# Kernel optimization log

Hardware: AMD Instinct MI355X
Metric: run time of the kernel (lower is better)

Reference implementation:

```python
import jax, jax.numpy as jnp
import numpy as np

N, G, E, B, H = 20000, 32768, 1_000_000, 64, 128

def _lin_w(k, fan_in, fan_out):
    return jax.random.normal(k, (fan_in, fan_out), jnp.float32) / np.sqrt(fan_in)

def setup_inputs() -> dict:
    key = jax.random.key(0)
    ks = jax.random.split(key, 12)
    node_embedding = jax.random.normal(ks[0], (N, H), jnp.float32)
    node_pos = jax.random.uniform(ks[1], (N, 3), jnp.float32)
    grid_pos = jax.random.uniform(ks[2], (G, 3), jnp.float32)
    index_i = jax.random.randint(ks[3], (E,), 0, N, jnp.int32)
    index_j = jax.random.randint(ks[4], (E,), N, N + G, jnp.int32)  # grid ids offset by N
    edge_index = jnp.stack([index_i, index_j], axis=0)
    # orthonormal per-graph frames via QR for realism
    q, _ = jnp.linalg.qr(jax.random.normal(ks[5], (B, 3, 3), jnp.float32))
    batch = jnp.sort(jax.random.randint(ks[6], (N,), 0, B, jnp.int32))
    wk = jax.random.split(ks[7], 6)
    return {
        "node_embedding": node_embedding, "node_pos": node_pos, "grid_pos": grid_pos,
        "edge_index": edge_index, "equi_frames": q, "batch": batch,
        "We1": _lin_w(wk[0], 3, H), "be1": jnp.zeros((H,), jnp.float32),
        "We2": _lin_w(wk[1], H, H), "be2": jnp.zeros((H,), jnp.float32),
        "Wm1": _lin_w(wk[2], 2 * H, H), "bm1": jnp.zeros((H,), jnp.float32),
        "Wm2": _lin_w(wk[3], H, H), "bm2": jnp.zeros((H,), jnp.float32),
        "Wu1": _lin_w(wk[4], H, H), "bu1": jnp.zeros((H,), jnp.float32),
        "Wu2": _lin_w(wk[5], H, H), "bu2": jnp.zeros((H,), jnp.float32),
    }

def _mlp(x, W1, b1, W2, b2):
    return jax.nn.silu(x @ W1 + b1) @ W2 + b2

def reference(node_embedding, node_pos, grid_pos, edge_index, equi_frames, batch,
              We1, be1, We2, be2, Wm1, bm1, Wm2, bm2, Wu1, bu1, Wu2, bu2):
    n_nodes = node_pos.shape[0]
    n_seg = n_nodes + grid_pos.shape[0]
    i, j = edge_index[0], edge_index[1]
    # per-edge gathers
    rel_pos = grid_pos[j - n_nodes] - node_pos[i]          # [E,3]
    frames = equi_frames[batch[i]]                          # [E,3,3]
    local_rel = jnp.einsum('eab,eb->ea', frames, rel_pos)   # frame bmm
    pos_emb = _mlp(local_rel, We1, be1, We2, be2)           # [E,H]
    msg = jnp.concatenate([node_embedding[i], pos_emb], -1) # [E,2H]
    msg = _mlp(msg, Wm1, bm1, Wm2, bm2)                     # [E,H]
    # scatter-mean over destination (grid) index; segments [0,N) receive none
    seg_sum = jax.ops.segment_sum(msg, j, num_segments=n_seg)
    cnt = jax.ops.segment_sum(jnp.ones((j.shape[0],), msg.dtype), j, num_segments=n_seg)
    mean = seg_sum / jnp.maximum(cnt, 1.0)[:, None]         # safe div (torch gives NaN on empty)
    return _mlp(mean, Wu1, bu1, Wu2, bu2)                   # [N+G, H]
```

## Files before the change

### kernel.cpp

```cpp
#include <hip/hip_runtime.h>
#include <hip/hip_fp16.h>

#define HN 128
#define NN 20000
#define GG 32768
#define EE 1000000
#define NSEG (NN + GG)
#define TE 128

typedef _Float16 f16;
typedef __attribute__((ext_vector_type(8))) _Float16 f16x8;
typedef __attribute__((ext_vector_type(4))) float f32x4;

__device__ __forceinline__ int swz_h(int row, int col) {
  int b = (row << 8) + (col << 1);
  b ^= (row & 7) << 4;
  return b >> 1;
}

__device__ __forceinline__ int swz_f(int row, int lcol) {
  int b = (row << 8) + (lcol << 2);
  b ^= (row & 7) << 4;
  return b >> 2;
}

__device__ __forceinline__ float silu_f(float x) {
  return x / (1.0f + __expf(-x));
}

__device__ __forceinline__ f32x4 mfma16(f16x8 a, f16x8 b, f32x4 c) {
  return __builtin_amdgcn_mfma_f32_16x16x32_f16(a, b, c, 0, 0, 0);
}

__global__ void pack_weights(const float* __restrict__ Wm1,
                             const float* __restrict__ Wm2,
                             const float* __restrict__ Wu1,
                             const float* __restrict__ Wu2,
                             f16* __restrict__ dst) {
  int p = blockIdx.x * 256 + threadIdx.x;
  if (p >= 81920) return;
  const float* src; int K, off, q;
  if (p < 32768)      { src = Wm1; K = 256; off = 0;     q = p; }
  else if (p < 49152) { src = Wm2; K = 128; off = 32768; q = p - 32768; }
  else if (p < 65536) { src = Wu1; K = 128; off = 49152; q = p - 49152; }
  else                { src = Wu2; K = 128; off = 65536; q = p - 65536; }
  int KS = K >> 5;
  int t   = q / (KS * 512);
  int rem = q - t * KS * 512;
  int s   = rem >> 9;
  int qq  = rem & 511;
  int lane = qq >> 3, e = qq & 7;
  int k = s * 32 + ((lane >> 4) << 3) + e;
  int n = (t << 4) + (lane & 15);
  dst[off + q] = (f16)src[k * HN + n];
}

__global__ void wc_vec_kernel(const float* __restrict__ We2,
                              const float* __restrict__ Wm1,
                              const float* __restrict__ be2,
                              const float* __restrict__ bm1,
                              const float* __restrict__ bu1,
                              const float* __restrict__ Wu2,
                              const float* __restrict__ bu2,
                              f16* __restrict__ Wcp,
                              float* __restrict__ bvec,
                              float* __restrict__ cvec) {
  if (blockIdx.x < 64) {
    int o = blockIdx.x * 256 + threadIdx.x;
    int k = o >> 7, n = o & 127;
    float s = 0.0f;
    for (int m = 0; m < 128; m++)
      s += We2[k * HN + m] * Wm1[(128 + m) * HN + n];
    int t = n >> 4, sg = k >> 5;
    int lane = (((k >> 3) & 3) << 4) | (n & 15);
    int e = k & 7;
    Wcp[((size_t)(t * 4 + sg) * 64 + lane) * 8 + e] = (f16)s;
  } else {
    int tid = threadIdx.x;
    if (tid < 128) {
      float s = bm1[tid];
      for (int m = 0; m < 128; m++) s += be2[m] * Wm1[(128 + m) * HN + tid];
      bvec[tid] = s;
    } else {
      int n = tid - 128;
      float s = bu2[n];
      for (int m = 0; m < 128; m++) s += silu_f(bu1[m]) * Wu2[m * HN + n];
      cvec[n] = s;
    }
  }
}

__global__ __launch_bounds__(256, 2) void ynode_kernel(
    const float* __restrict__ emb, const f16* __restrict__ Wm1p,
    const float* __restrict__ bvec, f16* __restrict__ Ynode) {
  __shared__ __align__(16) f16 A1[TE * HN];
  const int tid = threadIdx.x;
  const int rbase = blockIdx.x * TE;

  for (int idx = tid; idx < TE * HN; idx += 256) {
    int e = idx >> 7, h = idx & (HN - 1);
    int row = rbase + e;
    float v = (row < NN) ? emb[(size_t)row * HN + h] : 0.0f;
    A1[swz_h(e, h)] = (f16)v;
  }
  __syncthreads();

  const int lane = tid & 63;
  const int w = tid >> 6;
  const int lr_ = lane & 15;
  const int hi = lane >> 4;
  const int r0w = w * 32;

  f16x8 a[2][4];
#pragma unroll
  for (int mt = 0; mt < 2; mt++)
#pragma unroll
    for (int s = 0; s < 4; s++)
      a[mt][s] = *(const f16x8*)(A1 + swz_h(r0w + mt * 16 + lr_, s * 32 + hi * 8));

  f32x4 acc[2][8];
#pragma unroll
  for (int t = 0; t < 8; t++) {
    float bv = bvec[t * 16 + lr_];
    acc[0][t] = (f32x4){bv, bv, bv, bv};
    acc[1][t] = (f32x4){bv, bv, bv, bv};
  }
#pragma unroll
  for (int t = 0; t < 8; t++)
#pragma unroll
    for (int s = 0; s < 4; s++) {
      f16x8 b = *(const f16x8*)(Wm1p + (size_t)((t * 8 + s) * 64 + lane) * 8);
      acc[0][t] = mfma16(a[0][s], b, acc[0][t]);
      acc[1][t] = mfma16(a[1][s], b, acc[1][t]);
    }
#pragma unroll
  for (int mt = 0; mt < 2; mt++)
#pragma unroll
    for (int t = 0; t < 8; t++)
#pragma unroll
      for (int r = 0; r < 4; r++) {
        int row = rbase + r0w + mt * 16 + hi * 4 + r;
        if (row < NN)
          Ynode[(size_t)row * HN + t * 16 + lr_] = (f16)acc[mt][t][r];
      }
}

__global__ void hist_kernel(const int* __restrict__ eidx, int* __restrict__ hist) {
  int e = blockIdx.x * 256 + threadIdx.x;
  if (e < EE) atomicAdd(&hist[eidx[EE + e] - NN], 1);
}

__global__ __launch_bounds__(1024) void scan_kernel(const int* __restrict__ hist,
                                                    int* __restrict__ cursor) {
  __shared__ int sbuf[1024];
  int tid = threadIdx.x;
  int base = tid * 32;
  int v[32];
  int s = 0;
#pragma unroll
  for (int k = 0; k < 32; k++) { int t = hist[base + k]; v[k] = s; s += t; }
  int tot = s;
  sbuf[tid] = s;
  __syncthreads();
  for (int off = 1; off < 1024; off <<= 1) {
    int x = (tid >= off) ? sbuf[tid - off] : 0;
    __syncthreads();
    sbuf[tid] += x;
    __syncthreads();
  }
  int excl = sbuf[tid] - tot;
#pragma unroll
  for (int k = 0; k < 32; k++) cursor[base + k] = excl + v[k];
}

__global__ void reorder_kernel(const int* __restrict__ eidx,
                               int* __restrict__ cursor, int2* __restrict__ sij) {
  int e = blockIdx.x * 256 + threadIdx.x;
  if (e < EE) {
    int j = eidx[EE + e];
    int p = atomicAdd(&cursor[j - NN], 1);
    sij[p] = make_int2(eidx[e], j);
  }
}

__global__ __launch_bounds__(256, 3) void edge_kernel(
    const f16* __restrict__ Ynode, const float* __restrict__ npos,
    const float* __restrict__ gpos, const float* __restrict__ frames,
    const int* __restrict__ batch, const int2* __restrict__ sij,
    const float* __restrict__ We1, const float* __restrict__ be1,
    const f16* __restrict__ Wcp, float* __restrict__ out) {
  __shared__ __align__(16) float M[TE * 64];
  __shared__ float sW[4 * HN];
  __shared__ float sLR[TE * 3];
  __shared__ int sI[TE];
  __shared__ int sJ[TE];

  const int tid = threadIdx.x;
  const int ebase = blockIdx.x * TE;

  for (int k = tid; k < 4 * HN; k += 256)
    sW[k] = (k < 3 * HN) ? We1[k] : be1[k - 3 * HN];

  if (tid < TE) {
    int p = ebase + tid;
    bool valid = p < EE;
    int2 ij = sij[valid ? p : 0];
    int i = ij.x;
    int g = ij.y - NN;
    float r0 = gpos[g * 3 + 0] - npos[i * 3 + 0];
    float r1 = gpos[g * 3 + 1] - npos[i * 3 + 1];
    float r2 = gpos[g * 3 + 2] - npos[i * 3 + 2];
    const float* F = frames + batch[i] * 9;
    sLR[tid * 3 + 0] = F[0] * r0 + F[1] * r1 + F[2] * r2;
    sLR[tid * 3 + 1] = F[3] * r0 + F[4] * r1 + F[5] * r2;
    sLR[tid * 3 + 2] = F[6] * r0 + F[7] * r1 + F[8] * r2;
    sI[tid] = i;
    sJ[tid] = valid ? ij.y : -1;
  }
  __syncthreads();

  const int lane = tid & 63;
  const int w = tid >> 6;
  const int lr_ = lane & 15;
  const int hi = lane >> 4;
  const int r0w = w * 32;

  f16x8 afr[2][4];
#pragma unroll
  for (int mt = 0; mt < 2; mt++) {
    int row = r0w + mt * 16 + lr_;
    float l0 = sLR[row * 3 + 0], l1 = sLR[row * 3 + 1], l2 = sLR[row * 3 + 2];
#pragma unroll
    for (int s = 0; s < 4; s++) {
      f16x8 a;
#pragma unroll
      for (int e = 0; e < 8; e++) {
        int k = s * 32 + hi * 8 + e;
        float x = l0 * sW[k] + l1 * sW[HN + k] + l2 * sW[2 * HN + k] + sW[3 * HN + k];
        a[e] = (f16)silu_f(x);
      }
      afr[mt][s] = a;
    }
  }

  f32x4 acc[2][8];
#pragma unroll
  for (int mt = 0; mt < 2; mt++)
#pragma unroll
    for (int t = 0; t < 8; t++) acc[mt][t] = (f32x4){0.f, 0.f, 0.f, 0.f};
#pragma unroll
  for (int t = 0; t < 8; t++)
#pragma unroll
    for (int s = 0; s < 4; s++) {
      f16x8 b = *(const f16x8*)(Wcp + (size_t)((t * 4 + s) * 64 + lane) * 8);
      acc[0][t] = mfma16(afr[0][s], b, acc[0][t]);
      acc[1][t] = mfma16(afr[1][s], b, acc[1][t]);
    }

#pragma unroll
  for (int half = 0; half < 2; half++) {
    if (half) __syncthreads();
#pragma unroll
    for (int mt = 0; mt < 2; mt++)
#pragma unroll
      for (int tq = 0; tq < 4; tq++)
#pragma unroll
        for (int r = 0; r < 4; r++)
          M[swz_f(r0w + mt * 16 + hi * 4 + r, tq * 16 + lr_)] =
              acc[mt][half * 4 + tq][r];
    __syncthreads();
    const int colg = half * 64 + lane;
    f16 yv[32];
#pragma unroll
    for (int k = 0; k < 32; k++)
      yv[k] = Ynode[(size_t)sI[r0w + k] * HN + colg];
    float run = 0.0f;
    int jcur = -2;
#pragma unroll
    for (int k = 0; k < 32; k++) {
      int row = r0w + k;
      int jr = sJ[row];
      float v = silu_f(M[swz_f(row, lane)] + (float)yv[k]);
      if (jr != jcur) {
        if (jcur >= 0) atomicAdd(&out[(size_t)jcur * HN + colg], run);
        run = 0.0f;
        jcur = jr;
      }
      if (jr >= 0) run += v;
    }
    if (jcur >= 0) atomicAdd(&out[(size_t)jcur * HN + colg], run);
  }
}

__global__ __launch_bounds__(256, 2) void finalize_kernel(
    float* __restrict__ out, const int* __restrict__ hist,
    const f16* __restrict__ Wm2p, const float* __restrict__ bm2,
    const f16* __restrict__ Wu1p, const float* __restrict__ bu1,
    const f16* __restrict__ Wu2p, const float* __restrict__ bu2) {
  __shared__ __align__(16) f16 A1[TE * HN];
  __shared__ float sb[TE];
  const int tid = threadIdx.x;
  const int rbase = NN + blockIdx.x * TE;

  for (int idx = tid; idx < TE * HN; idx += 256) {
    int e = idx >> 7, h = idx & (HN - 1);
    int c = hist[rbase + e - NN];
    float v = out[(size_t)(rbase + e) * HN + h] / fmaxf((float)c, 1.0f);
    A1[swz_h(e, h)] = (f16)v;
    if (h == 0) sb[e] = (c > 0) ? 1.0f : 0.0f;
  }
  __syncthreads();

  const int lane = tid & 63;
  const int w = tid >> 6;
  const int lr_ = lane & 15;
  const int hi = lane >> 4;
  const int r0w = w * 32;

  f32x4 acc[2][8];

  {
    f16x8 a[2][4];
#pragma unroll
    for (int mt = 0; mt < 2; mt++)
#pragma unroll
      for (int s = 0; s < 4; s++)
        a[mt][s] = *(const f16x8*)(A1 + swz_h(r0w + mt * 16 + lr_, s * 32 + hi * 8));
#pragma unroll
    for (int mt = 0; mt < 2; mt++)
#pragma unroll
      for (int t = 0; t < 8; t++) {
        float bb = bm2[t * 16 + lr_];
        f32x4 c;
#pragma unroll
        for (int r = 0; r < 4; r++) c[r] = bb * sb[r0w + mt * 16 + hi * 4 + r];
        acc[mt][t] = c;
      }
#pragma unroll
    for (int t = 0; t < 8; t++)
#pragma unroll
      for (int s = 0; s < 4; s++) {
        f16x8 b = *(const f16x8*)(Wm2p + (size_t)((t * 4 + s) * 64 + lane) * 8);
        acc[0][t] = mfma16(a[0][s], b, acc[0][t]);
        acc[1][t] = mfma16(a[1][s], b, acc[1][t]);
      }
  }
  __syncthreads();
#pragma unroll
  for (int mt = 0; mt < 2; mt++)
#pragma unroll
    for (int t = 0; t < 8; t++)
#pragma unroll
      for (int r = 0; r < 4; r++)
        A1[swz_h(r0w + mt * 16 + hi * 4 + r, t * 16 + lr_)] = (f16)acc[mt][t][r];
  __syncthreads();

  {
    f16x8 a[2][4];
#pragma unroll
    for (int mt = 0; mt < 2; mt++)
#pragma unroll
      for (int s = 0; s < 4; s++)
        a[mt][s] = *(const f16x8*)(A1 + swz_h(r0w + mt * 16 + lr_, s * 32 + hi * 8));
#pragma unroll
    for (int t = 0; t < 8; t++) {
      float bv = bu1[t * 16 + lr_];
      acc[0][t] = (f32x4){bv, bv, bv, bv};
      acc[1][t] = (f32x4){bv, bv, bv, bv};
    }
#pragma unroll
    for (int t = 0; t < 8; t++)
#pragma unroll
      for (int s = 0; s < 4; s++) {
        f16x8 b = *(const f16x8*)(Wu1p + (size_t)((t * 4 + s) * 64 + lane) * 8);
        acc[0][t] = mfma16(a[0][s], b, acc[0][t]);
        acc[1][t] = mfma16(a[1][s], b, acc[1][t]);
      }
  }
  __syncthreads();
#pragma unroll
  for (int mt = 0; mt < 2; mt++)
#pragma unroll
    for (int t = 0; t < 8; t++)
#pragma unroll
      for (int r = 0; r < 4; r++)
        A1[swz_h(r0w + mt * 16 + hi * 4 + r, t * 16 + lr_)] = (f16)silu_f(acc[mt][t][r]);
  __syncthreads();

  {
    f16x8 a[2][4];
#pragma unroll
    for (int mt = 0; mt < 2; mt++)
#pragma unroll
      for (int s = 0; s < 4; s++)
        a[mt][s] = *(const f16x8*)(A1 + swz_h(r0w + mt * 16 + lr_, s * 32 + hi * 8));
#pragma unroll
    for (int t = 0; t < 8; t++) {
      float bv = bu2[t * 16 + lr_];
      acc[0][t] = (f32x4){bv, bv, bv, bv};
      acc[1][t] = (f32x4){bv, bv, bv, bv};
    }
#pragma unroll
    for (int t = 0; t < 8; t++)
#pragma unroll
      for (int s = 0; s < 4; s++) {
        f16x8 b = *(const f16x8*)(Wu2p + (size_t)((t * 4 + s) * 64 + lane) * 8);
        acc[0][t] = mfma16(a[0][s], b, acc[0][t]);
        acc[1][t] = mfma16(a[1][s], b, acc[1][t]);
      }
  }
#pragma unroll
  for (int mt = 0; mt < 2; mt++)
#pragma unroll
    for (int t = 0; t < 8; t++)
#pragma unroll
      for (int r = 0; r < 4; r++) {
        int row = rbase + r0w + mt * 16 + hi * 4 + r;
        out[(size_t)row * HN + t * 16 + lr_] = acc[mt][t][r];
      }
}

__global__ void constfill_kernel(const float* __restrict__ cvec,
                                 float* __restrict__ out) {
  int i = blockIdx.x * 256 + threadIdx.x;
  if (i < NN * HN / 4) {
    float4 v = reinterpret_cast<const float4*>(cvec)[i & 31];
    reinterpret_cast<float4*>(out)[i] = v;
  }
}

extern "C" void kernel_launch(void* const* d_in, const int* in_sizes, int n_in,
                              void* d_out, int out_size, void* d_ws, size_t ws_size,
                              hipStream_t stream) {
  const float* emb    = (const float*)d_in[0];
  const float* npos   = (const float*)d_in[1];
  const float* gpos   = (const float*)d_in[2];
  const int*   eidx   = (const int*)d_in[3];
  const float* frames = (const float*)d_in[4];
  const int*   batch  = (const int*)d_in[5];
  const float* We1 = (const float*)d_in[6];
  const float* be1 = (const float*)d_in[7];
  const float* We2 = (const float*)d_in[8];
  const float* be2 = (const float*)d_in[9];
  const float* Wm1 = (const float*)d_in[10];
  const float* bm1 = (const float*)d_in[11];
  const float* Wm2 = (const float*)d_in[12];
  const float* bm2 = (const float*)d_in[13];
  const float* Wu1 = (const float*)d_in[14];
  const float* bu1 = (const float*)d_in[15];
  const float* Wu2 = (const float*)d_in[16];
  const float* bu2 = (const float*)d_in[17];

  float* out  = (float*)d_out;
  char* ws    = (char*)d_ws;
  int* hist   = (int*)ws;
  int* cursor = (int*)(ws + 131072);
  f16* wp     = (f16*)(ws + 262144);
  f16* Wm1p   = wp;
  f16* Wm2p   = wp + 32768;
  f16* Wu1p   = wp + 49152;
  f16* Wu2p   = wp + 65536;
  f16* Wcp    = (f16*)(ws + 425984);
  float* bvec = (float*)(ws + 458752);
  float* cvec = (float*)(ws + 459264);
  int2* sij   = (int2*)(ws + 524288);
  f16* Ynode  = (f16*)(ws + 8524288);

  hipMemsetAsync(out + (size_t)NN * HN, 0, (size_t)GG * HN * sizeof(float), stream);
  hipMemsetAsync(hist, 0, (size_t)GG * sizeof(int), stream);

  pack_weights<<<320, 256, 0, stream>>>(Wm1, Wm2, Wu1, Wu2, wp);
  wc_vec_kernel<<<65, 256, 0, stream>>>(We2, Wm1, be2, bm1, bu1, Wu2, bu2,
                                        Wcp, bvec, cvec);
  ynode_kernel<<<(NN + TE - 1) / TE, 256, 0, stream>>>(emb, Wm1p, bvec, Ynode);

  int eb = (EE + 255) / 256;
  hist_kernel<<<eb, 256, 0, stream>>>(eidx, hist);
  scan_kernel<<<1, 1024, 0, stream>>>(hist, cursor);
  reorder_kernel<<<eb, 256, 0, stream>>>(eidx, cursor, sij);

  int eblocks = (EE + TE - 1) / TE;
  edge_kernel<<<eblocks, 256, 0, stream>>>(
      Ynode, npos, gpos, frames, batch, sij, We1, be1, Wcp, out);

  finalize_kernel<<<GG / TE, 256, 0, stream>>>(out, hist, Wm2p, bm2,
                                               Wu1p, bu1, Wu2p, bu2);
  constfill_kernel<<<(NN * HN / 4 + 255) / 256, 256, 0, stream>>>(cvec, out);
}
```

Measured before the change: 485.1 us.

## Merge prep kernels, fold constfill into finalize, restructure edge silu/Ynode add

Merges weight packing, combined-weight and bias precompute, and the edge histogram into one launch, and folds the constant fill for node rows into the finalize kernel. In the edge kernel, the Ynode gather and SiLU now happen in registers right after the MFMA instead of in the scatter loop, the position-embedding SiLU is computed with fused FMAs for both row tiles at once, and occupancy is raised to 4 blocks per CU. SiLU uses a hardware reciprocal instead of a division. The aim is fewer launches and less per-edge work, at the cost of register pressure and a slightly less accurate reciprocal.

```diff
diff --git a/kernel.cpp b/kernel.cpp
--- a/kernel.cpp
+++ b/kernel.cpp
@@ -25,129 +25,74 @@
 }
 
 __device__ __forceinline__ float silu_f(float x) {
-  return x / (1.0f + __expf(-x));
+  float d = 1.0f + __expf(-x);
+  return x * __builtin_amdgcn_rcpf(d);
 }
 
 __device__ __forceinline__ f32x4 mfma16(f16x8 a, f16x8 b, f32x4 c) {
   return __builtin_amdgcn_mfma_f32_16x16x32_f16(a, b, c, 0, 0, 0);
 }
 
-__global__ void pack_weights(const float* __restrict__ Wm1,
-                             const float* __restrict__ Wm2,
-                             const float* __restrict__ Wu1,
-                             const float* __restrict__ Wu2,
-                             f16* __restrict__ dst) {
-  int p = blockIdx.x * 256 + threadIdx.x;
-  if (p >= 81920) return;
-  const float* src; int K, off, q;
-  if (p < 32768)      { src = Wm1; K = 256; off = 0;     q = p; }
-  else if (p < 49152) { src = Wm2; K = 128; off = 32768; q = p - 32768; }
-  else if (p < 65536) { src = Wu1; K = 128; off = 49152; q = p - 49152; }
-  else                { src = Wu2; K = 128; off = 65536; q = p - 65536; }
-  int KS = K >> 5;
-  int t   = q / (KS * 512);
-  int rem = q - t * KS * 512;
-  int s   = rem >> 9;
-  int qq  = rem & 511;
-  int lane = qq >> 3, e = qq & 7;
-  int k = s * 32 + ((lane >> 4) << 3) + e;
-  int n = (t << 4) + (lane & 15);
-  dst[off + q] = (f16)src[k * HN + n];
-}
-
-__global__ void wc_vec_kernel(const float* __restrict__ We2,
-                              const float* __restrict__ Wm1,
-                              const float* __restrict__ be2,
-                              const float* __restrict__ bm1,
-                              const float* __restrict__ bu1,
-                              const float* __restrict__ Wu2,
-                              const float* __restrict__ bu2,
-                              f16* __restrict__ Wcp,
-                              float* __restrict__ bvec,
-                              float* __restrict__ cvec) {
-  if (blockIdx.x < 64) {
-    int o = blockIdx.x * 256 + threadIdx.x;
-    int k = o >> 7, n = o & 127;
-    float s = 0.0f;
-    for (int m = 0; m < 128; m++)
-      s += We2[k * HN + m] * Wm1[(128 + m) * HN + n];
-    int t = n >> 4, sg = k >> 5;
-    int lane = (((k >> 3) & 3) << 4) | (n & 15);
-    int e = k & 7;
-    Wcp[((size_t)(t * 4 + sg) * 64 + lane) * 8 + e] = (f16)s;
+__global__ void prep_kernel(const float* __restrict__ Wm1,
+                            const float* __restrict__ Wm2,
+                            const float* __restrict__ Wu1,
+                            const float* __restrict__ Wu2,
+                            const float* __restrict__ We2,
+                            const float* __restrict__ be2,
+                            const float* __restrict__ bm1,
+                            const float* __restrict__ bu1,
+                            const float* __restrict__ bu2,
+                            const int* __restrict__ eidx,
+                            f16* __restrict__ wp, f16* __restrict__ Wcp,
+                            float* __restrict__ bvec, float* __restrict__ cvec,
+                            int* __restrict__ hist) {
+  const int b = blockIdx.x;
+  const int tid = threadIdx.x;
+  if (b < 320) {
+    int p = b * 256 + tid;
+    if (p >= 81920) return;
+    const float* src; int K, off, q;
+    if (p < 32768)      { src = Wm1; K = 256; off = 0;     q = p; }
+    else if (p < 49152) { src = Wm2; K = 128; off = 32768; q = p - 32768; }
+    else if (p < 65536) { src = Wu1; K = 128; off = 49152; q = p - 49152; }
+    else                { src = Wu2; K = 128; off = 65536; q = p - 65536; }
+    int KS = K >> 5;
+    int t   = q / (KS * 512);
+    int rem = q - t * KS * 512;
+    int s   = rem >> 9;
+    int qq  = rem & 511;
+    int lane = qq >> 3, e = qq & 7;
+    int k = s * 32 + ((lane >> 4) << 3) + e;
+    int n = (t << 4) + (lane & 15);
+    wp[off + q] = (f16)src[k * HN + n];
+  } else if (b < 385) {
+    int bb = b - 320;
+    if (bb < 64) {
+      int o = bb * 256 + tid;
+      int k = o >> 7, n = o & 127;
+      float s = 0.0f;
+      for (int m = 0; m < 128; m++)
+        s += We2[k * HN + m] * Wm1[(128 + m) * HN + n];
+      int t = n >> 4, sg = k >> 5;
+      int lane = (((k >> 3) & 3) << 4) | (n & 15);
+      int e = k & 7;
+      Wcp[((size_t)(t * 4 + sg) * 64 + lane) * 8 + e] = (f16)s;
+    } else {
+      if (tid < 128) {
+        float s = bm1[tid];
+        for (int m = 0; m < 128; m++) s += be2[m] * Wm1[(128 + m) * HN + tid];
+        bvec[tid] = s;
+      } else {
+        int n = tid - 128;
+        float s = bu2[n];
+        for (int m = 0; m < 128; m++) s += silu_f(bu1[m]) * Wu2[m * HN + n];
+        cvec[n] = s;
+      }
+    }
   } else {
-    int tid = threadIdx.x;
-    if (tid < 128) {
-      float s = bm1[tid];
-      for (int m = 0; m < 128; m++) s += be2[m] * Wm1[(128 + m) * HN + tid];
-      bvec[tid] = s;
-    } else {
-      int n = tid - 128;
-      float s = bu2[n];
-      for (int m = 0; m < 128; m++) s += silu_f(bu1[m]) * Wu2[m * HN + n];
-      cvec[n] = s;
-    }
-  }
-}
-
-__global__ __launch_bounds__(256, 2) void ynode_kernel(
-    const float* __restrict__ emb, const f16* __restrict__ Wm1p,
-    const float* __restrict__ bvec, f16* __restrict__ Ynode) {
-  __shared__ __align__(16) f16 A1[TE * HN];
-  const int tid = threadIdx.x;
-  const int rbase = blockIdx.x * TE;
-
-  for (int idx = tid; idx < TE * HN; idx += 256) {
-    int e = idx >> 7, h = idx & (HN - 1);
-    int row = rbase + e;
-    float v = (row < NN) ? emb[(size_t)row * HN + h] : 0.0f;
-    A1[swz_h(e, h)] = (f16)v;
-  }
-  __syncthreads();
-
-  const int lane = tid & 63;
-  const int w = tid >> 6;
-  const int lr_ = lane & 15;
-  const int hi = lane >> 4;
-  const int r0w = w * 32;
-
-  f16x8 a[2][4];
-#pragma unroll
-  for (int mt = 0; mt < 2; mt++)
-#pragma unroll
-    for (int s = 0; s < 4; s++)
-      a[mt][s] = *(const f16x8*)(A1 + swz_h(r0w + mt * 16 + lr_, s * 32 + hi * 8));
-
-  f32x4 acc[2][8];
-#pragma unroll
-  for (int t = 0; t < 8; t++) {
-    float bv = bvec[t * 16 + lr_];
-    acc[0][t] = (f32x4){bv, bv, bv, bv};
-    acc[1][t] = (f32x4){bv, bv, bv, bv};
-  }
-#pragma unroll
-  for (int t = 0; t < 8; t++)
-#pragma unroll
-    for (int s = 0; s < 4; s++) {
-      f16x8 b = *(const f16x8*)(Wm1p + (size_t)((t * 8 + s) * 64 + lane) * 8);
-      acc[0][t] = mfma16(a[0][s], b, acc[0][t]);
-      acc[1][t] = mfma16(a[1][s], b, acc[1][t]);
-    }
-#pragma unroll
-  for (int mt = 0; mt < 2; mt++)
-#pragma unroll
-    for (int t = 0; t < 8; t++)
-#pragma unroll
-      for (int r = 0; r < 4; r++) {
-        int row = rbase + r0w + mt * 16 + hi * 4 + r;
-        if (row < NN)
-          Ynode[(size_t)row * HN + t * 16 + lr_] = (f16)acc[mt][t][r];
-      }
-}
-
-__global__ void hist_kernel(const int* __restrict__ eidx, int* __restrict__ hist) {
-  int e = blockIdx.x * 256 + threadIdx.x;
-  if (e < EE) atomicAdd(&hist[eidx[EE + e] - NN], 1);
+    int e = (b - 385) * 256 + tid;
+    if (e < EE) atomicAdd(&hist[eidx[EE + e] - NN], 1);
+  }
 }
 
 __global__ __launch_bounds__(1024) void scan_kernel(const int* __restrict__ hist,
@@ -183,7 +128,62 @@
   }
 }
 
-__global__ __launch_bounds__(256, 3) void edge_kernel(
+__global__ __launch_bounds__(256, 2) void ynode_kernel(
+    const float* __restrict__ emb, const f16* __restrict__ Wm1p,
+    const float* __restrict__ bvec, f16* __restrict__ Ynode) {
+  __shared__ __align__(16) f16 A1[TE * HN];
+  const int tid = threadIdx.x;
+  const int rbase = blockIdx.x * TE;
+
+  for (int idx = tid; idx < TE * HN; idx += 256) {
+    int e = idx >> 7, h = idx & (HN - 1);
+    int row = rbase + e;
+    float v = (row < NN) ? emb[(size_t)row * HN + h] : 0.0f;
+    A1[swz_h(e, h)] = (f16)v;
+  }
+  __syncthreads();
+
+  const int lane = tid & 63;
+  const int w = tid >> 6;
+  const int lr_ = lane & 15;
+  const int hi = lane >> 4;
+  const int r0w = w * 32;
+
+  f16x8 a[2][4];
+#pragma unroll
+  for (int mt = 0; mt < 2; mt++)
+#pragma unroll
+    for (int s = 0; s < 4; s++)
+      a[mt][s] = *(const f16x8*)(A1 + swz_h(r0w + mt * 16 + lr_, s * 32 + hi * 8));
+
+  f32x4 acc[2][8];
+#pragma unroll
+  for (int t = 0; t < 8; t++) {
+    float bv = bvec[t * 16 + lr_];
+    acc[0][t] = (f32x4){bv, bv, bv, bv};
+    acc[1][t] = (f32x4){bv, bv, bv, bv};
+  }
+#pragma unroll
+  for (int t = 0; t < 8; t++)
+#pragma unroll
+    for (int s = 0; s < 4; s++) {
+      f16x8 b = *(const f16x8*)(Wm1p + (size_t)((t * 8 + s) * 64 + lane) * 8);
+      acc[0][t] = mfma16(a[0][s], b, acc[0][t]);
+      acc[1][t] = mfma16(a[1][s], b, acc[1][t]);
+    }
+#pragma unroll
+  for (int mt = 0; mt < 2; mt++)
+#pragma unroll
+    for (int t = 0; t < 8; t++)
+#pragma unroll
+      for (int r = 0; r < 4; r++) {
+        int row = rbase + r0w + mt * 16 + hi * 4 + r;
+        if (row < NN)
+          Ynode[(size_t)row * HN + t * 16 + lr_] = (f16)acc[mt][t][r];
+      }
+}
+
+__global__ __launch_bounds__(256, 4) void edge_kernel(
     const f16* __restrict__ Ynode, const float* __restrict__ npos,
     const float* __restrict__ gpos, const float* __restrict__ frames,
     const int* __restrict__ batch, const int2* __restrict__ sij,
@@ -225,22 +225,21 @@
   const int hi = lane >> 4;
   const int r0w = w * 32;
 
+  const int row0 = r0w + lr_, row1 = r0w + 16 + lr_;
+  const float l00 = sLR[row0 * 3], l01 = sLR[row0 * 3 + 1], l02 = sLR[row0 * 3 + 2];
+  const float l10 = sLR[row1 * 3], l11 = sLR[row1 * 3 + 1], l12 = sLR[row1 * 3 + 2];
   f16x8 afr[2][4];
 #pragma unroll
-  for (int mt = 0; mt < 2; mt++) {
-    int row = r0w + mt * 16 + lr_;
-    float l0 = sLR[row * 3 + 0], l1 = sLR[row * 3 + 1], l2 = sLR[row * 3 + 2];
-#pragma unroll
-    for (int s = 0; s < 4; s++) {
-      f16x8 a;
-#pragma unroll
-      for (int e = 0; e < 8; e++) {
-        int k = s * 32 + hi * 8 + e;
-        float x = l0 * sW[k] + l1 * sW[HN + k] + l2 * sW[2 * HN + k] + sW[3 * HN + k];
-        a[e] = (f16)silu_f(x);
-      }
-      afr[mt][s] = a;
-    }
+  for (int s = 0; s < 4; s++) {
+    f16x8 a0, a1;
+#pragma unroll
+    for (int e = 0; e < 8; e++) {
+      int k = s * 32 + hi * 8 + e;
+      float w0 = sW[k], w1 = sW[HN + k], w2 = sW[2 * HN + k], wb = sW[3 * HN + k];
+      a0[e] = (f16)silu_f(fmaf(l02, w2, fmaf(l01, w1, fmaf(l00, w0, wb))));
+      a1[e] = (f16)silu_f(fmaf(l12, w2, fmaf(l11, w1, fmaf(l10, w0, wb))));
+    }
+    afr[0][s] = a0; afr[1][s] = a1;
   }
 
   f32x4 acc[2][8];
@@ -255,6 +254,17 @@
       f16x8 b = *(const f16x8*)(Wcp + (size_t)((t * 4 + s) * 64 + lane) * 8);
       acc[0][t] = mfma16(afr[0][s], b, acc[0][t]);
       acc[1][t] = mfma16(afr[1][s], b, acc[1][t]);
+    }
+
+  #pragma unroll
+  for (int mt = 0; mt < 2; mt++)
+#pragma unroll
+    for (int r = 0; r < 4; r++) {
+      int row = r0w + mt * 16 + hi * 4 + r;
+      const f16* yp = Ynode + (size_t)sI[row] * HN + lr_;
+#pragma unroll
+      for (int t = 0; t < 8; t++)
+        acc[mt][t][r] = silu_f(acc[mt][t][r] + (float)yp[t * 16]);
     }
 
 #pragma unroll
@@ -270,17 +280,13 @@
               acc[mt][half * 4 + tq][r];
     __syncthreads();
     const int colg = half * 64 + lane;
-    f16 yv[32];
-#pragma unroll
-    for (int k = 0; k < 32; k++)
-      yv[k] = Ynode[(size_t)sI[r0w + k] * HN + colg];
     float run = 0.0f;
     int jcur = -2;
 #pragma unroll
     for (int k = 0; k < 32; k++) {
       int row = r0w + k;
       int jr = sJ[row];
-      float v = silu_f(M[swz_f(row, lane)] + (float)yv[k]);
+      float v = M[swz_f(row, lane)];
       if (jr != jcur) {
         if (jcur >= 0) atomicAdd(&out[(size_t)jcur * HN + colg], run);
         run = 0.0f;
@@ -296,7 +302,8 @@
     float* __restrict__ out, const int* __restrict__ hist,
     const f16* __restrict__ Wm2p, const float* __restrict__ bm2,
     const f16* __restrict__ Wu1p, const float* __restrict__ bu1,
-    const f16* __restrict__ Wu2p, const float* __restrict__ bu2) {
+    const f16* __restrict__ Wu2p, const float* __restrict__ bu2,
+    const float* __restrict__ cvec) {
   __shared__ __align__(16) f16 A1[TE * HN];
   __shared__ float sb[TE];
   const int tid = threadIdx.x;
@@ -418,12 +425,8 @@
         int row = rbase + r0w + mt * 16 + hi * 4 + r;
         out[(size_t)row * HN + t * 16 + lr_] = acc[mt][t][r];
       }
-}
-
-__global__ void constfill_kernel(const float* __restrict__ cvec,
-                                 float* __restrict__ out) {
-  int i = blockIdx.x * 256 + threadIdx.x;
-  if (i < NN * HN / 4) {
+
+  for (int i = blockIdx.x * 256 + tid; i < NN * HN / 4; i += 256 * 256) {
     float4 v = reinterpret_cast<const float4*>(cvec)[i & 31];
     reinterpret_cast<float4*>(out)[i] = v;
   }
@@ -469,21 +472,19 @@
   hipMemsetAsync(out + (size_t)NN * HN, 0, (size_t)GG * HN * sizeof(float), stream);
   hipMemsetAsync(hist, 0, (size_t)GG * sizeof(int), stream);
 
-  pack_weights<<<320, 256, 0, stream>>>(Wm1, Wm2, Wu1, Wu2, wp);
-  wc_vec_kernel<<<65, 256, 0, stream>>>(We2, Wm1, be2, bm1, bu1, Wu2, bu2,
-                                        Wcp, bvec, cvec);
+  int hb = (EE + 255) / 256;
+  prep_kernel<<<385 + hb, 256, 0, stream>>>(
+      Wm1, Wm2, Wu1, Wu2, We2, be2, bm1, bu1, bu2, eidx,
+      wp, Wcp, bvec, cvec, hist);
+
+  scan_kernel<<<1, 1024, 0, stream>>>(hist, cursor);
+  reorder_kernel<<<hb, 256, 0, stream>>>(eidx, cursor, sij);
   ynode_kernel<<<(NN + TE - 1) / TE, 256, 0, stream>>>(emb, Wm1p, bvec, Ynode);
-
-  int eb = (EE + 255) / 256;
-  hist_kernel<<<eb, 256, 0, stream>>>(eidx, hist);
-  scan_kernel<<<1, 1024, 0, stream>>>(hist, cursor);
-  reorder_kernel<<<eb, 256, 0, stream>>>(eidx, cursor, sij);
 
   int eblocks = (EE + TE - 1) / TE;
   edge_kernel<<<eblocks, 256, 0, stream>>>(
       Ynode, npos, gpos, frames, batch, sij, We1, be1, Wcp, out);
 
   finalize_kernel<<<GG / TE, 256, 0, stream>>>(out, hist, Wm2p, bm2,
-                                               Wu1p, bu1, Wu2p, bu2);
-  constfill_kernel<<<(NN * HN / 4 + 255) / 256, 256, 0, stream>>>(cvec, out);
-}
+                                               Wu1p, bu1, Wu2p, bu2, cvec);
+}
```

Measured after the change: 409.2 us. 1.19x faster.
